# Optimization experiments

Hardware: AMD Instinct MI355X
Metric: run time of the kernel (lower is better)

Reference implementation:

```python
import jax, jax.numpy as jnp
import numpy as np
from jax import lax

B, T, H, C = 64, 512, 1024, 8


def setup_inputs() -> dict:
    key = jax.random.key(0)
    ks = jax.random.split(key, 7)
    encoding = jax.random.normal(ks[0], (B, T, H), dtype=jnp.float32)
    labels = jax.random.randint(ks[1], (B, 3 * T), 0, C)
    W = jax.random.normal(ks[2], (3, C, H), dtype=jnp.float32) * 0.02
    b = jax.random.normal(ks[3], (3, C), dtype=jnp.float32) * 0.02
    start_trans = jax.random.normal(ks[4], (3, C), dtype=jnp.float32) * 0.1
    end_trans = jax.random.normal(ks[5], (3, C), dtype=jnp.float32) * 0.1
    trans = jax.random.normal(ks[6], (3, C, C), dtype=jnp.float32) * 0.1
    return {"encoding": encoding, "labels": labels, "W": W, "b": b,
            "start_trans": start_trans, "end_trans": end_trans, "trans": trans}


def crf_neg_log_lik(em, tags, start, end, trans):
    # em [B,T,C], tags [B,T] -> scalar (torchcrf reduction='sum', loss = -llh)
    bsz = em.shape[0]
    # numerator: score of gold path
    em_sc = jnp.take_along_axis(em, tags[:, :, None], axis=2)[..., 0].sum(axis=1)
    tr_sc = trans[tags[:, :-1], tags[:, 1:]].sum(axis=1)
    num = start[tags[:, 0]] + em_sc + tr_sc + end[tags[:, -1]]
    # denominator: forward algorithm (log partition)
    a0 = start[None, :] + em[:, 0]  # [B,C]

    def step(a, e_t):
        a_new = jax.nn.logsumexp(a[:, :, None] + trans[None] + e_t[:, None, :], axis=1)
        return a_new, None

    aT, _ = lax.scan(step, a0, jnp.moveaxis(em[:, 1:], 1, 0))
    logZ = jax.nn.logsumexp(aT + end[None, :], axis=1)
    return -(num - logZ).sum()


def viterbi(em, start, end, trans):
    # em [B,T,C] -> best tag path [B,T] (no mask: all sequences full length)
    v0 = start[None, :] + em[:, 0]

    def step(v, e_t):
        s = v[:, :, None] + trans[None]          # [B,C_prev,C_cur]
        bp = jnp.argmax(s, axis=1)               # [B,C]
        return jnp.max(s, axis=1) + e_t, bp

    vT, bps = lax.scan(step, v0, jnp.moveaxis(em[:, 1:], 1, 0))  # bps [T-1,B,C]
    last = jnp.argmax(vT + end[None, :], axis=1)  # [B]

    def back(tag, bp):
        prev = jnp.take_along_axis(bp, tag[:, None], axis=1)[:, 0]
        return prev, prev

    _, rev = lax.scan(back, last, bps, reverse=True)  # [T-1,B], tags for t=0..T-2
    tags = jnp.concatenate([rev, last[None]], axis=0)  # [T,B]
    return tags.T


def reference(encoding, labels, W, b, start_trans, end_trans, trans):
    # three per-task projections: logits [3,B,T,C]
    logits = jnp.einsum('bth,kch->kbtc', encoding, W) + b[:, None, None, :]
    tags = jnp.stack(jnp.split(labels, 3, axis=1))  # [3,B,T] (task/process/material)
    losses = jax.vmap(crf_neg_log_lik)(logits, tags, start_trans, end_trans, trans)
    loss = losses.sum()
    pred = jax.vmap(viterbi)(logits, start_trans, end_trans, trans)  # [3,B,T]
    return loss, logits, pred
```

## Files before the change

kernel.cpp:

```cpp
#include <hip/hip_runtime.h>

#define NB 64
#define NT 512
#define NH 1024
#define NC 8
#define NK 3
#define BT (NB*NT)
#define LOGITS_N (NK*BT*NC)

#define QP1  0xB1
#define QP2  0x4E
#define ROR4 0x124
#define ROR8 0x128
#define HM   0x141

template<int CTRL>
__device__ __forceinline__ float dppf(float x) {
  return __int_as_float(__builtin_amdgcn_update_dpp(0, __float_as_int(x), CTRL, 0xF, 0xF, true));
}
template<int CTRL>
__device__ __forceinline__ int dppi(int x) {
  return __builtin_amdgcn_update_dpp(0, x, CTRL, 0xF, 0xF, true);
}

__device__ __forceinline__ void gload_lds16(const float* g, float* l) {
  __builtin_amdgcn_global_load_lds(
      (const __attribute__((address_space(1))) void*)g,
      (__attribute__((address_space(3))) void*)l, 16, 0, 0);
}

__global__ __launch_bounds__(256) void init_kernel(const float* __restrict__ W,
                                                   float* __restrict__ Wt,
                                                   float* __restrict__ out) {
  int i = blockIdx.x * 256 + threadIdx.x;
  if (i < 24 * NH) {
    int h = i / 24, j = i - h * 24;
    int kk = j >> 3, cc = j & 7;
    Wt[i] = W[kk * NC * NH + cc * NH + h];
  }
  if (i == 0) out[0] = 0.0f;
}

__global__ __launch_bounds__(256, 2) void proj_kernel(const float* __restrict__ enc,
                                                      const float* __restrict__ Wt,
                                                      const float* __restrict__ bias,
                                                      float* __restrict__ out) {
  __shared__ float smem[2 * 64 * 128];
  const int tid = threadIdx.x;
  const int lane = tid & 63;
  const int w = tid >> 6;
  const int row0 = blockIdx.x * 64;
  const int chrot = blockIdx.x & 7;
  const float* eb = enc + (size_t)row0 * 1024;

  float acc[24];
#pragma unroll
  for (int j = 0; j < 24; ++j) acc[j] = 0.0f;

  auto stage = [&](int ci, int buf) {
    const int cx = ci ^ chrot;
#pragma unroll
    for (int i = 0; i < 8; ++i) {
      const int r = w * 16 + 2 * i + (lane >> 5);
      const int s = (lane & 31) ^ (r & 7);
      const float* g = eb + (size_t)r * 1024 + cx * 128 + s * 4;
      gload_lds16(g, &smem[buf * 8192 + (w * 16 + 2 * i) * 128]);
    }
  };

  auto compute = [&](int ci, int buf) {
    const int cx = ci ^ chrot;
    const float* wbase = Wt + __builtin_amdgcn_readfirstlane((cx * 128 + w * 32) * 24);
    const float* er = &smem[buf * 8192 + lane * 128];
    const int rx = lane & 7;
#pragma unroll
    for (int hq = 0; hq < 8; ++hq) {
      const int slot = (w * 8 + hq) ^ rx;
      const float4 e4 = *(const float4*)&er[slot * 4];
      const float ev[4] = {e4.x, e4.y, e4.z, e4.w};
      const float* wr = wbase + hq * 96;
#pragma unroll
      for (int m = 0; m < 4; ++m) {
        const float e = ev[m];
        const float* wm = wr + m * 24;
#pragma unroll
        for (int j = 0; j < 24; ++j) acc[j] = fmaf(e, wm[j], acc[j]);
      }
    }
  };

  stage(0, 0);

#pragma unroll 1
  for (int ci = 0; ci < 8; ++ci) {
    const int buf = ci & 1;
    if (ci < 7) {
      stage(ci + 1, buf ^ 1);
      asm volatile("s_waitcnt vmcnt(8)" ::: "memory");
    } else {
      asm volatile("s_waitcnt vmcnt(0)" ::: "memory");
    }
    __builtin_amdgcn_s_barrier();
    asm volatile("" ::: "memory");
    compute(ci, buf);
    asm volatile("" ::: "memory");
    __builtin_amdgcn_s_barrier();
  }

  float* sp = smem + w * 1792;
#pragma unroll
  for (int j4 = 0; j4 < 24; j4 += 4)
    *(float4*)&sp[lane * 28 + j4] = make_float4(acc[j4], acc[j4+1], acc[j4+2], acc[j4+3]);
  __syncthreads();
  const int r = tid >> 2, j0 = (tid & 3) * 6;
#pragma unroll
  for (int u = 0; u < 6; ++u) {
    const int j = j0 + u;
    float s = smem[0 * 1792 + r * 28 + j] + smem[1 * 1792 + r * 28 + j]
            + smem[2 * 1792 + r * 28 + j] + smem[3 * 1792 + r * 28 + j] + bias[j];
    out[1 + (size_t)(j >> 3) * (BT * 8) + (size_t)(row0 + r) * 8 + (j & 7)] = s;
  }
}

__global__ __launch_bounds__(512) void crf_kernel(const int* __restrict__ labels,
                                                  const float* __restrict__ startT,
                                                  const float* __restrict__ endT,
                                                  const float* __restrict__ trans,
                                                  float* __restrict__ d_out) {
  __shared__ float sA[32 * 64];
  __shared__ float sVB[32 * 8];
  __shared__ int   sBP[512];
  __shared__ int   sMap[32 * 8];
  __shared__ int   sEnt[32];
  __shared__ float sRed[32];
  __shared__ unsigned char sTags[512];
  __shared__ int sTerm;

  const int tid = threadIdx.x;
  const int lane = tid & 63;
  const int w = tid >> 6;
  const int c = lane & 7;
  const int p = (lane >> 3) & 7;
  const int role = (blockIdx.x >= 192);
  const int seq = role ? blockIdx.x - 192 : blockIdx.x;
  const int k = seq >> 6, b = seq & 63;
  const float* em = d_out + 1 + ((size_t)k * BT + (size_t)b * 512) * 8;
  const float* trk = trans + k * 64;
  const int* lab = labels + b * (NK * NT) + k * NT;

  float Txc[8];
#pragma unroll
  for (int kk = 0; kk < 8; ++kk) Txc[kk] = trk[(c ^ kk) * 8 + c];
  const float Tpc = trk[p * 8 + c];
  const float startc = startT[k * 8 + c];
  const float endc = endT[k * 8 + c];

  if (!role) {
    float Mxc[8];
#pragma unroll
    for (int kk = 0; kk < 8; ++kk) Mxc[kk] = __expf(Txc[kk]);

#pragma unroll 1
    for (int it = 0; it < 4; ++it) {
      const int i = w * 4 + it;
      const int t0 = i * 16;
      const int te = (t0 + 16 < 512) ? (t0 + 16) : 511;
      float EX[16];
      EX[0] = em[(t0 + 1) * 8 + c];
#pragma unroll
      for (int j = 1; j < 16; ++j) {
        int t = t0 + 1 + j;
        EX[j] = (t <= te) ? __expf(em[t * 8 + c]) : 1.0f;
      }
      float V = __expf(Tpc + EX[0]);
#pragma unroll
      for (int j = 1; j < 16; ++j) {
        int t = t0 + 1 + j;
        if (t <= te) {
          float x1 = dppf<QP1>(V), x2 = dppf<QP2>(V), x3 = dppf<QP2>(x1);
          float x7 = dppf<HM>(V), x6 = dppf<QP1>(x7), x5 = dppf<QP2>(x7), x4 = dppf<QP2>(x6);
          float s01 = fmaf(x1, Mxc[1], V * Mxc[0]);
          float s23 = fmaf(x3, Mxc[3], x2 * Mxc[2]);
          float s45 = fmaf(x5, Mxc[5], x4 * Mxc[4]);
          float s67 = fmaf(x7, Mxc[7], x6 * Mxc[6]);
          V = ((s01 + s23) + (s45 + s67)) * EX[j];
        }
        if (j == 8) V *= 0x1p-32f;
      }
      sA[i * 64 + lane] = V;
    }
    __syncthreads();

    float logZ = 0.0f;
    if (w == 0) {
      float al = __expf(startc + em[c]);
      float lz = 0.0f;
#pragma unroll 1
      for (int i = 0; i < 32; ++i) {
        const float* Ai = &sA[i * 64];
        float A0 = Ai[(c ^ 0) * 8 + c], A1 = Ai[(c ^ 1) * 8 + c];
        float A2 = Ai[(c ^ 2) * 8 + c], A3 = Ai[(c ^ 3) * 8 + c];
        float A4 = Ai[(c ^ 4) * 8 + c], A5 = Ai[(c ^ 5) * 8 + c];
        float A6 = Ai[(c ^ 6) * 8 + c], A7 = Ai[(c ^ 7) * 8 + c];
        float a1 = dppf<QP1>(al), a2 = dppf<QP2>(al), a3 = dppf<QP2>(a1);
        float a4 = dppf<ROR4>(al), a5 = dppf<ROR4>(a1), a6 = dppf<ROR4>(a2), a7 = dppf<ROR4>(a3);
        float s01 = fmaf(a1, A1, al * A0);
        float s23 = fmaf(a3, A3, a2 * A2);
        float s45 = fmaf(a5, A5, a4 * A4);
        float s67 = fmaf(a7, A7, a6 * A6);
        float s = (s01 + s23) + (s45 + s67);
        float ss = s;
        ss += dppf<QP1>(ss); ss += dppf<QP2>(ss); ss += dppf<ROR4>(ss);
        lz += __logf(ss);
        al = s * (1.0f / ss);
      }
      float se = al * __expf(endc);
      se += dppf<QP1>(se); se += dppf<QP2>(se); se += dppf<ROR4>(se);
      logZ = lz + __logf(se) + 1024.0f * 0.69314718055994531f;
    } else {
      int idx = (w - 1) * 64 + lane;
      float ns = 0.0f;
      {
        int tg = lab[idx];
        ns += em[(size_t)idx * 8 + tg] + trk[tg * 8 + lab[idx + 1]];
      }
      if (idx < 64) {
        int t = idx + 448;
        int tg = lab[t];
        ns += em[(size_t)t * 8 + tg];
        if (t < 511) ns += trk[tg * 8 + lab[t + 1]];
      }
      ns += dppf<QP1>(ns); ns += dppf<QP2>(ns); ns += dppf<HM>(ns); ns += dppf<ROR8>(ns);
      if ((lane & 15) == 0) sRed[(w - 1) * 4 + (lane >> 4)] = ns;
    }
    __syncthreads();
    if (tid == 0) {
      float num = startT[k * 8 + lab[0]] + endT[k * 8 + lab[511]];
#pragma unroll
      for (int u = 0; u < 28; ++u) num += sRed[u];
      atomicAdd(d_out, logZ - num);
    }
  } else {
#pragma unroll 1
    for (int it = 0; it < 4; ++it) {
      const int i = w * 4 + it;
      const int t0 = i * 16;
      const int te = (t0 + 16 < 512) ? (t0 + 16) : 511;
      float emv[16];
#pragma unroll
      for (int j = 0; j < 16; ++j) {
        int t = t0 + 1 + j;
        emv[j] = (t <= te) ? em[t * 8 + c] : 0.0f;
      }
      float V = Tpc + emv[0];
#pragma unroll
      for (int j = 1; j < 16; ++j) {
        int t = t0 + 1 + j;
        if (t <= te) {
          float x1 = dppf<QP1>(V), x2 = dppf<QP2>(V), x3 = dppf<QP2>(x1);
          float x7 = dppf<HM>(V), x6 = dppf<QP1>(x7), x5 = dppf<QP2>(x7), x4 = dppf<QP2>(x6);
          float c0 = V + Txc[0], c1 = x1 + Txc[1], c2 = x2 + Txc[2], c3 = x3 + Txc[3];
          float c4 = x4 + Txc[4], c5 = x5 + Txc[5], c6 = x6 + Txc[6], c7 = x7 + Txc[7];
          float m0 = fmaxf(fmaxf(c0, c1), c2);
          float m1 = fmaxf(fmaxf(c3, c4), c5);
          float m2 = fmaxf(c6, c7);
          V = fmaxf(fmaxf(m0, m1), m2) + emv[j];
        }
      }
      sA[i * 64 + lane] = V;
    }
    __syncthreads();

    if (w == 0) {
      float v = startc + em[c];
#pragma unroll 1
      for (int i = 0; i < 32; ++i) {
        if (lane < 8) sVB[i * 8 + c] = v;
        const float* Ai = &sA[i * 64];
        float A0 = Ai[(c ^ 0) * 8 + c], A1 = Ai[(c ^ 1) * 8 + c];
        float A2 = Ai[(c ^ 2) * 8 + c], A3 = Ai[(c ^ 3) * 8 + c];
        float A4 = Ai[(c ^ 4) * 8 + c], A5 = Ai[(c ^ 5) * 8 + c];
        float A6 = Ai[(c ^ 6) * 8 + c], A7 = Ai[(c ^ 7) * 8 + c];
        float a1 = dppf<QP1>(v), a2 = dppf<QP2>(v), a3 = dppf<QP2>(a1);
        float a4 = dppf<ROR4>(v), a5 = dppf<ROR4>(a1), a6 = dppf<ROR4>(a2), a7 = dppf<ROR4>(a3);
        float c0 = v + A0, c1 = a1 + A1, c2 = a2 + A2, c3 = a3 + A3;
        float c4 = a4 + A4, c5 = a5 + A5, c6 = a6 + A6, c7 = a7 + A7;
        float m0 = fmaxf(fmaxf(c0, c1), c2);
        float m1 = fmaxf(fmaxf(c3, c4), c5);
        float m2 = fmaxf(c6, c7);
        v = fmaxf(fmaxf(m0, m1), m2);
      }
      float lv = v + endc;
      int li = c;
      {
        float ov; int oi; bool take;
        ov = dppf<QP1>(lv); oi = dppi<QP1>(li);
        take = (ov > lv) || (ov == lv && oi < li); lv = take ? ov : lv; li = take ? oi : li;
        ov = dppf<QP2>(lv); oi = dppi<QP2>(li);
        take = (ov > lv) || (ov == lv && oi < li); lv = take ? ov : lv; li = take ? oi : li;
        ov = dppf<ROR4>(lv); oi = dppi<ROR4>(li);
        take = (ov > lv) || (ov == lv && oi < li); lv = take ? ov : lv; li = take ? oi : li;
      }
      if (lane == 0) sTerm = li;
    }
    __syncthreads();

    if (w < 4) {
      const int u = lane >> 3;
      const int i = w * 8 + u;
      const int t0 = i * 16;
      const int te = (t0 + 16 < 512) ? (t0 + 16) : 511;
      float emv[16];
#pragma unroll
      for (int j = 0; j < 16; ++j) {
        int t = t0 + 1 + j;
        emv[j] = (t <= te) ? em[t * 8 + c] : 0.0f;
      }
      float v = sVB[i * 8 + c];
#pragma unroll
      for (int j = 0; j < 16; ++j) {
        int t = t0 + 1 + j;
        if (t <= te) {
          float x1 = dppf<QP1>(v), x2 = dppf<QP2>(v), x3 = dppf<QP2>(x1);
          float x7 = dppf<HM>(v), x6 = dppf<QP1>(x7), x5 = dppf<QP2>(x7), x4 = dppf<QP2>(x6);
          float c0 = v + Txc[0], c1 = x1 + Txc[1], c2 = x2 + Txc[2], c3 = x3 + Txc[3];
          float c4 = x4 + Txc[4], c5 = x5 + Txc[5], c6 = x6 + Txc[6], c7 = x7 + Txc[7];
          float m0 = fmaxf(fmaxf(c0, c1), c2);
          float m1 = fmaxf(fmaxf(c3, c4), c5);
          float m2 = fmaxf(c6, c7);
          float best = fmaxf(fmaxf(m0, m1), m2);
          int a0 = (c0 == best) ? (c ^ 0) : 8;
          int a1i = (c1 == best) ? (c ^ 1) : 8;
          int a2i = (c2 == best) ? (c ^ 2) : 8;
          int a3i = (c3 == best) ? (c ^ 3) : 8;
          int a4i = (c4 == best) ? (c ^ 4) : 8;
          int a5i = (c5 == best) ? (c ^ 5) : 8;
          int a6i = (c6 == best) ? (c ^ 6) : 8;
          int a7i = (c7 == best) ? (c ^ 7) : 8;
          int arg = min(min(min(a0, a1i), min(a2i, a3i)),
                        min(min(a4i, a5i), min(a6i, a7i)));
          v = best + emv[j];
          int wd = arg << (3 * c);
          wd |= dppi<QP1>(wd); wd |= dppi<QP2>(wd); wd |= dppi<HM>(wd);
          if ((lane & 7) == 0) sBP[t] = wd;
        }
      }
    }
    __syncthreads();

    if (w < 4) {
      const int u = lane >> 3;
      const int i = w * 8 + u;
      const int t0 = i * 16;
      const int te = (t0 + 16 < 512) ? (t0 + 16) : 511;
      int tag = c;
#pragma unroll
      for (int j = 16; j >= 1; --j) {
        int t = t0 + j;
        if (t <= te) tag = (sBP[t] >> (3 * tag)) & 7;
      }
      sMap[i * 8 + c] = tag;
    }
    __syncthreads();
    if (tid == 0) {
      int cur = sTerm;
#pragma unroll 1
      for (int i = 31; i >= 0; --i) { cur = sMap[i * 8 + cur]; sEnt[i] = cur; }
    }
    __syncthreads();
    if (w == 0 && lane < 32) {
      const int i = lane;
      const int t0 = i * 16;
      const int te = (t0 + 16 < 512) ? (t0 + 16) : 511;
      int tag = (i == 31) ? sTerm : sEnt[i + 1];
      if (i == 31) sTags[511] = (unsigned char)tag;
#pragma unroll
      for (int j = 16; j >= 1; --j) {
        int t = t0 + j;
        if (t <= te) { tag = (sBP[t] >> (3 * tag)) & 7; sTags[t - 1] = (unsigned char)tag; }
      }
    }
    __syncthreads();
    float* outp = d_out + 1 + LOGITS_N + (size_t)seq * 512;
    outp[tid] = (float)sTags[tid];
  }
}

extern "C" void kernel_launch(void* const* d_in, const int* in_sizes, int n_in,
                              void* d_out, int out_size, void* d_ws, size_t ws_size,
                              hipStream_t stream) {
  const float* enc    = (const float*)d_in[0];
  const int*   labels = (const int*)  d_in[1];
  const float* W      = (const float*)d_in[2];
  const float* bias   = (const float*)d_in[3];
  const float* startT = (const float*)d_in[4];
  const float* endT   = (const float*)d_in[5];
  const float* trans  = (const float*)d_in[6];
  float* out = (float*)d_out;
  float* Wt  = (float*)d_ws;

  init_kernel<<<dim3(96), dim3(256), 0, stream>>>(W, Wt, out);
  proj_kernel<<<dim3(512), dim3(256), 0, stream>>>(enc, Wt, bias, out);
  crf_kernel<<<dim3(384), dim3(512), 0, stream>>>(labels, startT, endT, trans, out);
}
```

Baseline: 268.3 us.

## Retile projection kernel to 128-row blocks with two rows per lane

```diff
diff --git a/kernel.cpp b/kernel.cpp
--- a/kernel.cpp
+++ b/kernel.cpp
@@ -41,50 +41,54 @@
   if (i == 0) out[0] = 0.0f;
 }
 
-__global__ __launch_bounds__(256, 2) void proj_kernel(const float* __restrict__ enc,
+__global__ __launch_bounds__(512, 1) void proj_kernel(const float* __restrict__ enc,
                                                       const float* __restrict__ Wt,
                                                       const float* __restrict__ bias,
                                                       float* __restrict__ out) {
-  __shared__ float smem[2 * 64 * 128];
+  __shared__ float smem[25600];
   const int tid = threadIdx.x;
   const int lane = tid & 63;
   const int w = tid >> 6;
-  const int row0 = blockIdx.x * 64;
-  const int chrot = blockIdx.x & 7;
+  const int row0 = blockIdx.x * 128;
   const float* eb = enc + (size_t)row0 * 1024;
 
-  float acc[24];
-#pragma unroll
-  for (int j = 0; j < 24; ++j) acc[j] = 0.0f;
+  float acc0[24], acc1[24];
+#pragma unroll
+  for (int j = 0; j < 24; ++j) { acc0[j] = 0.0f; acc1[j] = 0.0f; }
 
   auto stage = [&](int ci, int buf) {
-    const int cx = ci ^ chrot;
-#pragma unroll
-    for (int i = 0; i < 8; ++i) {
-      const int r = w * 16 + 2 * i + (lane >> 5);
-      const int s = (lane & 31) ^ (r & 7);
-      const float* g = eb + (size_t)r * 1024 + cx * 128 + s * 4;
-      gload_lds16(g, &smem[buf * 8192 + (w * 16 + 2 * i) * 128]);
+#pragma unroll
+    for (int i = 0; i < 4; ++i) {
+      const int rbase = w * 16 + i * 4;
+      const int r = rbase + (lane >> 4);
+      const int s = (lane & 15) ^ (r & 7);
+      gload_lds16(eb + (size_t)r * 1024 + ci * 64 + s * 4,
+                  &smem[buf * 8192 + rbase * 64]);
     }
   };
 
   auto compute = [&](int ci, int buf) {
-    const int cx = ci ^ chrot;
-    const float* wbase = Wt + __builtin_amdgcn_readfirstlane((cx * 128 + w * 32) * 24);
-    const float* er = &smem[buf * 8192 + lane * 128];
-    const int rx = lane & 7;
-#pragma unroll
-    for (int hq = 0; hq < 8; ++hq) {
-      const int slot = (w * 8 + hq) ^ rx;
-      const float4 e4 = *(const float4*)&er[slot * 4];
-      const float ev[4] = {e4.x, e4.y, e4.z, e4.w};
-      const float* wr = wbase + hq * 96;
+    const float* wp = Wt + __builtin_amdgcn_readfirstlane((ci * 64 + w * 8) * 24);
+    const int sw = lane & 7;
+    const float* r0 = &smem[buf * 8192 + lane * 64];
+    const float* r1 = r0 + 4096;
+#pragma unroll
+    for (int t = 0; t < 2; ++t) {
+      const int sl = (((w * 2 + t) ^ sw)) * 4;
+      const float4 e0 = *(const float4*)&r0[sl];
+      const float4 e1 = *(const float4*)&r1[sl];
+      const float ev0[4] = {e0.x, e0.y, e0.z, e0.w};
+      const float ev1[4] = {e1.x, e1.y, e1.z, e1.w};
+      const float* wt4 = wp + t * 96;
 #pragma unroll
       for (int m = 0; m < 4; ++m) {
-        const float e = ev[m];
-        const float* wm = wr + m * 24;
-#pragma unroll
-        for (int j = 0; j < 24; ++j) acc[j] = fmaf(e, wm[j], acc[j]);
+        const float a = ev0[m], b = ev1[m];
+        const float* wc = wt4 + m * 24;
+#pragma unroll
+        for (int j = 0; j < 24; ++j) {
+          acc0[j] = fmaf(a, wc[j], acc0[j]);
+          acc1[j] = fmaf(b, wc[j], acc1[j]);
+        }
       }
     }
   };
@@ -92,33 +96,31 @@
   stage(0, 0);
 
 #pragma unroll 1
-  for (int ci = 0; ci < 8; ++ci) {
+  for (int ci = 0; ci < 16; ++ci) {
     const int buf = ci & 1;
-    if (ci < 7) {
-      stage(ci + 1, buf ^ 1);
-      asm volatile("s_waitcnt vmcnt(8)" ::: "memory");
-    } else {
-      asm volatile("s_waitcnt vmcnt(0)" ::: "memory");
-    }
-    __builtin_amdgcn_s_barrier();
-    asm volatile("" ::: "memory");
+    __syncthreads();
+    if (ci < 15) stage(ci + 1, buf ^ 1);
     compute(ci, buf);
-    asm volatile("" ::: "memory");
-    __builtin_amdgcn_s_barrier();
   }
 
-  float* sp = smem + w * 1792;
-#pragma unroll
-  for (int j4 = 0; j4 < 24; j4 += 4)
-    *(float4*)&sp[lane * 28 + j4] = make_float4(acc[j4], acc[j4+1], acc[j4+2], acc[j4+3]);
   __syncthreads();
-  const int r = tid >> 2, j0 = (tid & 3) * 6;
-#pragma unroll
-  for (int u = 0; u < 6; ++u) {
-    const int j = j0 + u;
-    float s = smem[0 * 1792 + r * 28 + j] + smem[1 * 1792 + r * 28 + j]
-            + smem[2 * 1792 + r * 28 + j] + smem[3 * 1792 + r * 28 + j] + bias[j];
-    out[1 + (size_t)(j >> 3) * (BT * 8) + (size_t)(row0 + r) * 8 + (j & 7)] = s;
+  {
+    float* p0 = &smem[w * 3200 + lane * 25];
+    float* p1 = p0 + 64 * 25;
+#pragma unroll
+    for (int j = 0; j < 24; ++j) { p0[j] = acc0[j]; p1[j] = acc1[j]; }
+  }
+  __syncthreads();
+  {
+    const int row = tid >> 2, j0 = (tid & 3) * 6;
+#pragma unroll
+    for (int u = 0; u < 6; ++u) {
+      const int j = j0 + u;
+      float s = bias[j];
+#pragma unroll
+      for (int w8 = 0; w8 < 8; ++w8) s += smem[w8 * 3200 + row * 25 + j];
+      out[1 + (size_t)(j >> 3) * (BT * 8) + (size_t)(row0 + row) * 8 + (j & 7)] = s;
+    }
   }
 }
 
@@ -400,6 +402,6 @@
   float* Wt  = (float*)d_ws;
 
   init_kernel<<<dim3(96), dim3(256), 0, stream>>>(W, Wt, out);
-  proj_kernel<<<dim3(512), dim3(256), 0, stream>>>(enc, Wt, bias, out);
+  proj_kernel<<<dim3(256), dim3(512), 0, stream>>>(enc, Wt, bias, out);
   crf_kernel<<<dim3(384), dim3(512), 0, stream>>>(labels, startT, endT, trans, out);
 }
```

Result: faster. 251.7 us (-6.2%).
